# Kernel tuning notes

Hardware: AMD Instinct MI355X
Metric: run time of the kernel (lower is better)

## Reference

```python
import jax, jax.numpy as jnp
import numpy as np

NUM_EMB = 1024
EMB_DIM = 32


def setup_inputs() -> dict:
    key = jax.random.key(0)
    k1, k2 = jax.random.split(key)
    z = jax.random.normal(k1, (32, EMB_DIM, 64, 64), dtype=jnp.float32)
    # nn.Embedding weight init: uniform(-1/num_embeddings, 1/num_embeddings)
    emb_weight = jax.random.uniform(
        k2, (NUM_EMB, EMB_DIM), dtype=jnp.float32,
        minval=-1.0 / NUM_EMB, maxval=1.0 / NUM_EMB)
    return {"z": z, "emb_weight": emb_weight}


def reference(z, emb_weight):
    # z: [B, C, H, W] -> [B, H, W, C]
    z_p = jnp.transpose(z, (0, 2, 3, 1))
    B, H, W, C = z_p.shape
    z_flat = z_p.reshape(-1, C)  # [N, C]
    # squared distances via expansion: ||z||^2 + ||e||^2 - 2 z.e  -> [N, K]
    d = (jnp.sum(z_flat * z_flat, axis=1, keepdims=True)
         + jnp.sum(emb_weight * emb_weight, axis=1)
         - 2.0 * jnp.matmul(z_flat, emb_weight.T))
    idx = jnp.argmin(d, axis=1)  # [N]
    z_q = emb_weight[idx].reshape(B, H, W, C)
    # straight-through estimator (applied in BHWC, then back to BCHW)
    z_q = z_p + jax.lax.stop_gradient(z_q - z_p)
    z_q = jnp.transpose(z_q, (0, 3, 1, 2))  # [B, C, H, W]
    return z_q, idx
```

## Files before the change

### kernel.cpp

```cpp
#include <hip/hip_runtime.h>


#define NUM_EMB 1024
#define EMB_DIM 32
#define HW      4096
#define BATCH   32
#define N_TOT   (BATCH * HW)
#define NSPLIT  4
#define CODES_PER (NUM_EMB / NSPLIT)
#define MARGIN  1.0e-4f
#define CHUNK   256

#define OFF_BQ    0u
#define OFF_EH    4096u
#define WS_NEED   69632u
#define WS_NEED_R7 (4096u + 4u * 131072u * 8u)

using f16x8 = __attribute__((ext_vector_type(8))) _Float16;
using f32x4 = __attribute__((ext_vector_type(4))) float;

#define REPEAT32(M) \
    M(0)  M(1)  M(2)  M(3)  M(4)  M(5)  M(6)  M(7)  \
    M(8)  M(9)  M(10) M(11) M(12) M(13) M(14) M(15) \
    M(16) M(17) M(18) M(19) M(20) M(21) M(22) M(23) \
    M(24) M(25) M(26) M(27) M(28) M(29) M(30) M(31)

__device__ __forceinline__ float pairwise_sq32(const float* __restrict__ e) {
    float r0 = __fmul_rn(e[0], e[0]), r1 = __fmul_rn(e[1], e[1]);
    float r2 = __fmul_rn(e[2], e[2]), r3 = __fmul_rn(e[3], e[3]);
    float r4 = __fmul_rn(e[4], e[4]), r5 = __fmul_rn(e[5], e[5]);
    float r6 = __fmul_rn(e[6], e[6]), r7 = __fmul_rn(e[7], e[7]);
#pragma unroll
    for (int i = 8; i < 32; i += 8) {
        r0 = __fadd_rn(r0, __fmul_rn(e[i + 0], e[i + 0]));
        r1 = __fadd_rn(r1, __fmul_rn(e[i + 1], e[i + 1]));
        r2 = __fadd_rn(r2, __fmul_rn(e[i + 2], e[i + 2]));
        r3 = __fadd_rn(r3, __fmul_rn(e[i + 3], e[i + 3]));
        r4 = __fadd_rn(r4, __fmul_rn(e[i + 4], e[i + 4]));
        r5 = __fadd_rn(r5, __fmul_rn(e[i + 5], e[i + 5]));
        r6 = __fadd_rn(r6, __fmul_rn(e[i + 6], e[i + 6]));
        r7 = __fadd_rn(r7, __fmul_rn(e[i + 7], e[i + 7]));
    }
    return __fadd_rn(__fadd_rn(__fadd_rn(r0, r1), __fadd_rn(r2, r3)),
                     __fadd_rn(__fadd_rn(r4, r5), __fadd_rn(r6, r7)));
}

__device__ __forceinline__ void store_row16(unsigned short* dst,
                                            const unsigned short* v) {
    unsigned w[16];
#pragma unroll
    for (int i = 0; i < 16; ++i)
        w[i] = (unsigned)v[2 * i] | ((unsigned)v[2 * i + 1] << 16);
    uint4* d4 = (uint4*)dst;
    d4[0] = make_uint4(w[0], w[1], w[2], w[3]);
    d4[1] = make_uint4(w[4], w[5], w[6], w[7]);
    d4[2] = make_uint4(w[8], w[9], w[10], w[11]);
    d4[3] = make_uint4(w[12], w[13], w[14], w[15]);
}

__global__ __launch_bounds__(256) void vq_prep_e(
        const float* __restrict__ emb, float* __restrict__ bq,
        unsigned short* __restrict__ eh) {
    const int g = blockIdx.x * 256 + threadIdx.x;
    if (g >= NUM_EMB) return;
    const float* e = emb + g * EMB_DIM;
    bq[g] = pairwise_sq32(e);
    unsigned short h[32];
#pragma unroll
    for (int c = 0; c < 32; ++c) {
        _Float16 hv = (_Float16)(-2.0f * e[c]);
        h[c] = __builtin_bit_cast(unsigned short, hv);
    }
    store_row16(eh + (size_t)g * 32, h);
}

#define LOADZ(c) float z##c = zp[(size_t)(c) * HW];
#define Z_SQ_A()                                                              \
    float r0 = __fmul_rn(z0, z0), r1 = __fmul_rn(z1, z1);                     \
    float r2 = __fmul_rn(z2, z2), r3 = __fmul_rn(z3, z3);                     \
    float r4 = __fmul_rn(z4, z4), r5 = __fmul_rn(z5, z5);                     \
    float r6 = __fmul_rn(z6, z6), r7 = __fmul_rn(z7, z7);                     \
    r0 = __fadd_rn(r0, __fmul_rn(z8,  z8));  r0 = __fadd_rn(r0, __fmul_rn(z16, z16)); \
    r0 = __fadd_rn(r0, __fmul_rn(z24, z24));                                  \
    r1 = __fadd_rn(r1, __fmul_rn(z9,  z9));  r1 = __fadd_rn(r1, __fmul_rn(z17, z17)); \
    r1 = __fadd_rn(r1, __fmul_rn(z25, z25));                                  \
    r2 = __fadd_rn(r2, __fmul_rn(z10, z10)); r2 = __fadd_rn(r2, __fmul_rn(z18, z18)); \
    r2 = __fadd_rn(r2, __fmul_rn(z26, z26));                                  \
    r3 = __fadd_rn(r3, __fmul_rn(z11, z11)); r3 = __fadd_rn(r3, __fmul_rn(z19, z19)); \
    r3 = __fadd_rn(r3, __fmul_rn(z27, z27));                                  \
    r4 = __fadd_rn(r4, __fmul_rn(z12, z12)); r4 = __fadd_rn(r4, __fmul_rn(z20, z20)); \
    r4 = __fadd_rn(r4, __fmul_rn(z28, z28));                                  \
    r5 = __fadd_rn(r5, __fmul_rn(z13, z13)); r5 = __fadd_rn(r5, __fmul_rn(z21, z21)); \
    r5 = __fadd_rn(r5, __fmul_rn(z29, z29));                                  \
    r6 = __fadd_rn(r6, __fmul_rn(z14, z14)); r6 = __fadd_rn(r6, __fmul_rn(z22, z22)); \
    r6 = __fadd_rn(r6, __fmul_rn(z30, z30));                                  \
    r7 = __fadd_rn(r7, __fmul_rn(z15, z15)); r7 = __fadd_rn(r7, __fmul_rn(z23, z23)); \
    r7 = __fadd_rn(r7, __fmul_rn(z31, z31));                                  \
    const float a = __fadd_rn(                                                \
        __fadd_rn(__fadd_rn(r0, r1), __fadd_rn(r2, r3)),                      \
        __fadd_rn(__fadd_rn(r4, r5), __fadd_rn(r6, r7)));

#define FMA1(k) m = __fmaf_rn(z##k, e[(k)], m);
#define EXACT_KEY(jv)                                                         \
    {                                                                         \
        const float* e = emb + (size_t)(jv) * EMB_DIM;                        \
        float m = 0.0f;                                                       \
        REPEAT32(FMA1)                                                        \
        float d = __fsub_rn(__fadd_rn(a, bq[(jv)]), __fmul_rn(2.0f, m));      \
        unsigned u = __float_as_uint(d);                                      \
        u = (u & 0x80000000u) ? ~u : (u | 0x80000000u);                       \
        unsigned long long kk =                                               \
            ((unsigned long long)u << 32) | (unsigned)(jv);                   \
        if (kk < bestk) bestk = kk;                                           \
    }

__global__ __launch_bounds__(256, 4) void vq_filter(
        const float* __restrict__ z, const float* __restrict__ emb,
        const unsigned short* __restrict__ eh,
        const float* __restrict__ bq,
        float* __restrict__ out_zq, float* __restrict__ out_idx) {
    __shared__ __align__(16) char smem[17408];
    __shared__ int snB;
    int* scand  = (int*)smem;
    int* sdest  = (int*)(smem + 1024);
    int* sBlist = (int*)(smem + 1280);
    unsigned long long* bs =
        (unsigned long long*)(smem + 1536);

    const int tid  = threadIdx.x;
    const int lane = tid & 63;
    const int wv   = tid >> 6;
    const int cloc = lane & 15, quad = lane >> 4;
    const int q  = blockIdx.x * 64 + wv * 16 + cloc;
    const int b  = q >> 12;
    const int hw = q & 4095;

    f16x8 az;
    {
        const float* zb = z + ((size_t)b * EMB_DIM + quad * 8) * HW + hw;
#pragma unroll
        for (int k = 0; k < 8; ++k)
            az[k] = (_Float16)zb[(size_t)k * HW];
    }

    float m1[4], m2[4];
#pragma unroll
    for (int r = 0; r < 4; ++r) { m1[r] = 3.4e38f; m2[r] = 3.4e38f; }
    const unsigned km = 0xFFFFFFC0u;
    const int fbase = cloc * 64 + quad * 16;

    for (int ch = 0; ch < 4; ++ch) {
        if (ch) __syncthreads();
        {
            const uint4* src = (const uint4*)(eh + (size_t)ch * CHUNK * 32);
            uint4* dst = (uint4*)smem;
#pragma unroll
            for (int i = 0; i < 4; ++i) dst[i * 256 + tid] = src[i * 256 + tid];
            ((float*)(smem + 16384))[tid] = bq[ch * CHUNK + tid];
        }
        __syncthreads();

        float c1[4], c2[4];
#pragma unroll
        for (int r = 0; r < 4; ++r) { c1[r] = 3.4e38f; c2[r] = 3.4e38f; }
        const float* sb = (const float*)(smem + 16384);

#pragma unroll
        for (int jt = 0; jt < 16; ++jt) {
            f16x8 ef = *(const f16x8*)(smem + fbase + jt * 1024);
            const float bqv = sb[jt * 16 + cloc];
            f32x4 acc = {bqv, bqv, bqv, bqv};
            acc = __builtin_amdgcn_mfma_f32_16x16x32_f16(az, ef, acc, 0, 0, 0);
#pragma unroll
            for (int r = 0; r < 4; ++r) {
                const float kv = __uint_as_float(
                    (__float_as_uint(acc[r]) & km) | (unsigned)jt);
                c2[r] = __builtin_amdgcn_fmed3f(kv, c1[r], c2[r]);
                c1[r] = fminf(c1[r], kv);
            }
        }

        const unsigned chb = (unsigned)ch << 4;
#pragma unroll
        for (int r = 0; r < 4; ++r) {
            const float a1 = __uint_as_float(__float_as_uint(c1[r]) | chb);
            const float a2 = __uint_as_float(__float_as_uint(c2[r]) | chb);
            m2[r] = fminf(fmaxf(m1[r], a1), fminf(m2[r], a2));
            m1[r] = fminf(m1[r], a1);
        }
    }
    __syncthreads();

    float g[4];
#pragma unroll
    for (int r = 0; r < 4; ++r) g[r] = m1[r];
#pragma unroll
    for (int off = 1; off < 16; off <<= 1)
#pragma unroll
        for (int r = 0; r < 4; ++r)
            g[r] = fminf(g[r], __shfl_xor(g[r], off, 64));

#pragma unroll
    for (int r = 0; r < 4; ++r) {
        const float thr = g[r] + MARGIN;
        const int   ql  = wv * 16 + quad * 4 + r;
        const bool  f1  = m1[r] <= thr;
        const bool  f2  = m2[r] <= thr;
        const unsigned long long b1 = __ballot(f1);
        const unsigned long long b2 = __ballot(f2);
        const unsigned mk1 = (unsigned)(b1 >> (quad * 16)) & 0xFFFFu;
        const unsigned mk2 = (unsigned)(b2 >> (quad * 16)) & 0xFFFFu;
        const int pc  = __popc(mk1);
        const int ldr = __ffs(mk1) - 1;
        if (mk2 | (unsigned)(pc > 4)) {
            if (cloc == ldr) sdest[ql] = 5;
        } else {
            if (f1)
                scand[(ql << 2) + __popc(mk1 & ((1u << cloc) - 1u))] =
                    (int)(__float_as_uint(m1[r]) & 63u) * 16 + cloc;
            if (cloc == ldr) sdest[ql] = pc;
        }
    }
    __syncthreads();

    int d = 0, myidx = 0;
    if (tid < 64) {
        d = sdest[tid];
        const unsigned long long mB = __ballot(d == 5);
        if (tid == 0) snB = (int)__popcll(mB);
        if (d == 5) {
            sBlist[(int)__popcll(mB & ((1ull << lane) - 1ull))] = tid;
        } else if (d == 1) {
            myidx = scand[tid << 2];
        } else {
            const int n  = blockIdx.x * 64 + tid;
            const int bb = n >> 12;
            const int hh = n & 4095;
            const float* zp = z + (size_t)bb * EMB_DIM * HW + hh;
            REPEAT32(LOADZ)
            Z_SQ_A()
            unsigned long long bestk = ~0ull;
            for (int k = 0; k < d; ++k) {
                const int jv = scand[(tid << 2) + k];
                EXACT_KEY(jv)
            }
            myidx = (int)(unsigned)(bestk & 0xffffffffu);
        }
    }
    __syncthreads();

    if (tid < 64 && d != 5) {
        const int n = blockIdx.x * 64 + tid;
        out_idx[n] = (float)myidx;
        const int bb = n >> 12;
        const int hh = n & 4095;
        const float4* er = (const float4*)(emb + (size_t)myidx * EMB_DIM);
        float* op = out_zq + (size_t)bb * EMB_DIM * HW + hh;
#pragma unroll
        for (int c4 = 0; c4 < 8; ++c4) {
            float4 v = er[c4];
            op[(size_t)(c4 * 4 + 0) * HW] = v.x;
            op[(size_t)(c4 * 4 + 1) * HW] = v.y;
            op[(size_t)(c4 * 4 + 2) * HW] = v.z;
            op[(size_t)(c4 * 4 + 3) * HW] = v.w;
        }
    }

    const int nB = snB;
    for (int ib = 0; ib < nB; ++ib) {
        const int ql = sBlist[ib];
        const int n  = blockIdx.x * 64 + ql;
        const int bb = n >> 12;
        const int hh = n & 4095;
        const float* zp = z + (size_t)bb * EMB_DIM * HW + hh;
        REPEAT32(LOADZ)
        Z_SQ_A()
        unsigned long long bestk = ~0ull;
#pragma unroll
        for (int k = 0; k < 4; ++k) { const int jv = tid * 4 + k; EXACT_KEY(jv) }
        bs[tid] = bestk;
        __syncthreads();
        for (int off = 128; off > 0; off >>= 1) {
            if (tid < off && bs[tid + off] < bs[tid]) bs[tid] = bs[tid + off];
            __syncthreads();
        }
        const int fb = (int)(unsigned)(bs[0] & 0xffffffffu);
        if (tid == 0) out_idx[n] = (float)fb;
        if (tid < EMB_DIM)
            out_zq[(size_t)bb * EMB_DIM * HW + (size_t)tid * HW + hh] =
                emb[(size_t)fb * EMB_DIM + tid];
        __syncthreads();
    }
}

#define SCAN_GROUP4(j)                                                        \
    {                                                                         \
        const float* e = emb + (size_t)(j) * EMB_DIM;                         \
        const float bq0 = bq[(j) + 0], bq1 = bq[(j) + 1];                     \
        const float bq2 = bq[(j) + 2], bq3 = bq[(j) + 3];                     \
        float m0 = 0.0f, m1 = 0.0f, m2 = 0.0f, m3 = 0.0f;                     \
        REPEAT32(FMA_K)                                                       \
        float d0 = __fsub_rn(__fadd_rn(a, bq0), __fmul_rn(2.0f, m0));         \
        float d1 = __fsub_rn(__fadd_rn(a, bq1), __fmul_rn(2.0f, m1));         \
        float d2 = __fsub_rn(__fadd_rn(a, bq2), __fmul_rn(2.0f, m2));         \
        float d3 = __fsub_rn(__fadd_rn(a, bq3), __fmul_rn(2.0f, m3));         \
        if (d0 < best) { best = d0; bidx = (j) + 0; }                         \
        if (d1 < best) { best = d1; bidx = (j) + 1; }                         \
        if (d2 < best) { best = d2; bidx = (j) + 2; }                         \
        if (d3 < best) { best = d3; bidx = (j) + 3; }                         \
    }
#define FMA_K(k) \
        m0 = __fmaf_rn(z##k, e[0 * EMB_DIM + (k)], m0); \
        m1 = __fmaf_rn(z##k, e[1 * EMB_DIM + (k)], m1); \
        m2 = __fmaf_rn(z##k, e[2 * EMB_DIM + (k)], m2); \
        m3 = __fmaf_rn(z##k, e[3 * EMB_DIM + (k)], m3);

__global__ __launch_bounds__(256) void vq_sqnorm_kernel(
        const float* __restrict__ emb, float* __restrict__ bq) {
    int j = blockIdx.x * 256 + threadIdx.x;
    if (j < NUM_EMB) bq[j] = pairwise_sq32(emb + j * EMB_DIM);
}

__global__ __launch_bounds__(128, 4) void vq_partial_kernel(
        const float* __restrict__ z, const float* __restrict__ emb,
        const float* __restrict__ bq, unsigned long long* __restrict__ pk) {
    const int n  = blockIdx.x * 128 + threadIdx.x;
    const int b  = n >> 12;
    const int hw = n & 4095;
    const float* zp = z + (size_t)b * EMB_DIM * HW + hw;
    REPEAT32(LOADZ)
    Z_SQ_A()
    const int j0 = blockIdx.y * CODES_PER;
    float best = 3.4e38f;
    int   bidx = j0;
    for (int j = j0; j < j0 + CODES_PER; j += 4) SCAN_GROUP4(j)
    pk[(size_t)blockIdx.y * N_TOT + n] =
        ((unsigned long long)__float_as_uint(best) << 32) | (unsigned)bidx;
}

__global__ __launch_bounds__(256, 2) void vq_main_kernel(
        const float* __restrict__ z, const float* __restrict__ emb,
        const float* __restrict__ bq, float* __restrict__ out_zq,
        float* __restrict__ out_idx) {
    const int n  = blockIdx.x * 256 + threadIdx.x;
    const int b  = n >> 12;
    const int hw = n & 4095;
    const float* zp = z + (size_t)b * EMB_DIM * HW + hw;
    REPEAT32(LOADZ)
    Z_SQ_A()
    float best = 3.4e38f;
    int   bidx = 0;
    for (int j = 0; j < NUM_EMB; j += 4) SCAN_GROUP4(j)
    out_idx[n] = (float)bidx;
    const float* eb = emb + (size_t)bidx * EMB_DIM;
    float* op = out_zq + (size_t)b * EMB_DIM * HW + hw;
#pragma unroll
    for (int cc = 0; cc < EMB_DIM; ++cc) op[(size_t)cc * HW] = eb[cc];
}

__global__ __launch_bounds__(256) void vq_combine_kernel(
        const float* __restrict__ emb,
        const unsigned long long* __restrict__ pk,
        float* __restrict__ out_zq, float* __restrict__ out_idx) {
    const int n = blockIdx.x * 256 + threadIdx.x;
    unsigned long long m = pk[n];
#pragma unroll
    for (int y = 1; y < NSPLIT; ++y) {
        unsigned long long v = pk[(size_t)y * N_TOT + n];
        if (v < m) m = v;
    }
    const int bidx = (int)(unsigned)(m & 0xffffffffu);
    out_idx[n] = (float)bidx;
    const int b  = n >> 12;
    const int hw = n & 4095;
    const float* eb = emb + (size_t)bidx * EMB_DIM;
    float* op = out_zq + (size_t)b * EMB_DIM * HW + hw;
#pragma unroll
    for (int cc = 0; cc < EMB_DIM; ++cc) op[(size_t)cc * HW] = eb[cc];
}

extern "C" void kernel_launch(void* const* d_in, const int* in_sizes, int n_in,
                              void* d_out, int out_size, void* d_ws,
                              size_t ws_size, hipStream_t stream) {
    const float* z   = (const float*)d_in[0];
    const float* emb = (const float*)d_in[1];
    char* ws = (char*)d_ws;
    float* out0 = (float*)d_out;
    float* out1 = out0 + (size_t)BATCH * EMB_DIM * HW;

    if (ws_size >= WS_NEED) {
        float*          bq = (float*)(ws + OFF_BQ);
        unsigned short* eh = (unsigned short*)(ws + OFF_EH);

        vq_prep_e<<<4, 256, 0, stream>>>(emb, bq, eh);
        vq_filter<<<N_TOT / 64, 256, 0, stream>>>(z, emb, eh, bq,
                                                  out0, out1);
    } else if (ws_size >= WS_NEED_R7) {
        float* bq = (float*)ws;
        unsigned long long* pk = (unsigned long long*)(ws + 4096);
        vq_sqnorm_kernel<<<NUM_EMB / 256, 256, 0, stream>>>(emb, bq);
        vq_partial_kernel<<<dim3(N_TOT / 128, NSPLIT), 128, 0, stream>>>(
            z, emb, bq, pk);
        vq_combine_kernel<<<N_TOT / 256, 256, 0, stream>>>(emb, pk, out0, out1);
    } else {
        float* bq = (float*)ws;
        vq_sqnorm_kernel<<<NUM_EMB / 256, 256, 0, stream>>>(emb, bq);
        vq_main_kernel<<<N_TOT / 256, 256, 0, stream>>>(z, emb, bq, out0, out1);
    }
}
```

Measured before the change: 136.2 us.

## Stream fp16 codebook from global/L2 with register prefetch instead of LDS staging

Removes the four-chunk LDS staging of the half-precision codebook and its barriers. Each wave now reads codebook fragments and bias values straight from global memory, with a four-deep register prefetch pipeline over 64 code tiles, and keeps one running top-2 per row instead of per-chunk merging. The goal is to drop LDS copy and __syncthreads overhead and cut shared memory use so more blocks can be resident. The cost is repeated global/L2 traffic, since each wave reloads the same 64KB codebook, and exposed load latency if the prefetch depth is too shallow.

```diff
diff --git a/kernel.cpp b/kernel.cpp
--- a/kernel.cpp
+++ b/kernel.cpp
@@ -9,7 +9,6 @@
 #define NSPLIT  4
 #define CODES_PER (NUM_EMB / NSPLIT)
 #define MARGIN  1.0e-4f
-#define CHUNK   256
 
 #define OFF_BQ    0u
 #define OFF_EH    4096u
@@ -114,18 +113,29 @@
         if (kk < bestk) bestk = kk;                                           \
     }
 
+#define SBODY(EF, BQV, JTV)                                                   \
+    {                                                                         \
+        f32x4 acc = {(BQV), (BQV), (BQV), (BQV)};                             \
+        acc = __builtin_amdgcn_mfma_f32_16x16x32_f16(az, (EF), acc, 0, 0, 0); \
+        _Pragma("unroll")                                                     \
+        for (int r = 0; r < 4; ++r) {                                         \
+            const float kv = __uint_as_float(                                 \
+                (__float_as_uint(acc[r]) & km) | (unsigned)(JTV));            \
+            m2[r] = __builtin_amdgcn_fmed3f(kv, m1[r], m2[r]);                \
+            m1[r] = fminf(m1[r], kv);                                         \
+        }                                                                     \
+    }
+
 __global__ __launch_bounds__(256, 4) void vq_filter(
         const float* __restrict__ z, const float* __restrict__ emb,
         const unsigned short* __restrict__ eh,
         const float* __restrict__ bq,
         float* __restrict__ out_zq, float* __restrict__ out_idx) {
-    __shared__ __align__(16) char smem[17408];
+    __shared__ int scand[256];
+    __shared__ int sdest[64];
+    __shared__ int sBlist[64];
+    __shared__ unsigned long long bs[256];
     __shared__ int snB;
-    int* scand  = (int*)smem;
-    int* sdest  = (int*)(smem + 1024);
-    int* sBlist = (int*)(smem + 1280);
-    unsigned long long* bs =
-        (unsigned long long*)(smem + 1536);
 
     const int tid  = threadIdx.x;
     const int lane = tid & 63;
@@ -146,50 +156,33 @@
     float m1[4], m2[4];
 #pragma unroll
     for (int r = 0; r < 4; ++r) { m1[r] = 3.4e38f; m2[r] = 3.4e38f; }
+
     const unsigned km = 0xFFFFFFC0u;
-    const int fbase = cloc * 64 + quad * 16;
-
-    for (int ch = 0; ch < 4; ++ch) {
-        if (ch) __syncthreads();
-        {
-            const uint4* src = (const uint4*)(eh + (size_t)ch * CHUNK * 32);
-            uint4* dst = (uint4*)smem;
-#pragma unroll
-            for (int i = 0; i < 4; ++i) dst[i * 256 + tid] = src[i * 256 + tid];
-            ((float*)(smem + 16384))[tid] = bq[ch * CHUNK + tid];
-        }
-        __syncthreads();
-
-        float c1[4], c2[4];
-#pragma unroll
-        for (int r = 0; r < 4; ++r) { c1[r] = 3.4e38f; c2[r] = 3.4e38f; }
-        const float* sb = (const float*)(smem + 16384);
-
-#pragma unroll
-        for (int jt = 0; jt < 16; ++jt) {
-            f16x8 ef = *(const f16x8*)(smem + fbase + jt * 1024);
-            const float bqv = sb[jt * 16 + cloc];
-            f32x4 acc = {bqv, bqv, bqv, bqv};
-            acc = __builtin_amdgcn_mfma_f32_16x16x32_f16(az, ef, acc, 0, 0, 0);
-#pragma unroll
-            for (int r = 0; r < 4; ++r) {
-                const float kv = __uint_as_float(
-                    (__float_as_uint(acc[r]) & km) | (unsigned)jt);
-                c2[r] = __builtin_amdgcn_fmed3f(kv, c1[r], c2[r]);
-                c1[r] = fminf(c1[r], kv);
-            }
-        }
-
-        const unsigned chb = (unsigned)ch << 4;
-#pragma unroll
-        for (int r = 0; r < 4; ++r) {
-            const float a1 = __uint_as_float(__float_as_uint(c1[r]) | chb);
-            const float a2 = __uint_as_float(__float_as_uint(c2[r]) | chb);
-            m2[r] = fminf(fmaxf(m1[r], a1), fminf(m2[r], a2));
-            m1[r] = fminf(m1[r], a1);
-        }
-    }
-    __syncthreads();
+    const char* efp = (const char*)eh + cloc * 64 + quad * 16;
+    const float* bqp = bq + cloc;
+
+    f16x8 ef0 = *(const f16x8*)(efp + 0 * 1024);
+    f16x8 ef1 = *(const f16x8*)(efp + 1 * 1024);
+    f16x8 ef2 = *(const f16x8*)(efp + 2 * 1024);
+    f16x8 ef3 = *(const f16x8*)(efp + 3 * 1024);
+    float bq0 = bqp[0 * 16], bq1 = bqp[1 * 16];
+    float bq2 = bqp[2 * 16], bq3 = bqp[3 * 16];
+
+#pragma unroll 1
+    for (int jt = 0; jt < 60; jt += 4) {
+        SBODY(ef0, bq0, jt + 0)
+        ef0 = *(const f16x8*)(efp + (jt + 4) * 1024); bq0 = bqp[(jt + 4) * 16];
+        SBODY(ef1, bq1, jt + 1)
+        ef1 = *(const f16x8*)(efp + (jt + 5) * 1024); bq1 = bqp[(jt + 5) * 16];
+        SBODY(ef2, bq2, jt + 2)
+        ef2 = *(const f16x8*)(efp + (jt + 6) * 1024); bq2 = bqp[(jt + 6) * 16];
+        SBODY(ef3, bq3, jt + 3)
+        ef3 = *(const f16x8*)(efp + (jt + 7) * 1024); bq3 = bqp[(jt + 7) * 16];
+    }
+    SBODY(ef0, bq0, 60)
+    SBODY(ef1, bq1, 61)
+    SBODY(ef2, bq2, 62)
+    SBODY(ef3, bq3, 63)
 
     float g[4];
 #pragma unroll
```

Result: slower. 148.1 us (+8.7%).
